# Optimization experiments

Hardware: AMD Instinct MI355X
Metric: run time of the kernel (lower is better)

The kernel has to match this reference:

```python
import jax, jax.numpy as jnp
import numpy as np

B, NQ, NP_, D = 4, 2048, 8192, 256
T, H = 10, 4  # num_tables, num_hash_functions -> hash code length T*H = 40


def setup_inputs() -> dict:
    key = jax.random.key(0)
    k1, k2, k3 = jax.random.split(key, 3)
    return {
        "query_points": jax.random.normal(k1, (B, NQ, D), dtype=jnp.float32),
        "points": jax.random.normal(k2, (B, NP_, D), dtype=jnp.float32),
        "proj": jax.random.normal(k3, (T * H, D), dtype=jnp.float32),  # projection_matrices
        "k": 16,
    }


def _hash(x, proj):
    # x: [B, N, D], proj: [T*H, D] -> binary hash [B, N, T*H]
    return (jnp.einsum('bnd,fd->bnf', x, proj) > 0).astype(jnp.float32)


def reference(query_points, points, proj, k):
    qh = _hash(query_points, proj)   # [B, Nq, F]
    ph = _hash(points, proj)         # [B, Np, F]
    # L1 cdist on {0,1}-valued vectors == Hamming: |a-b| = a + b - 2ab (exact in fp32).
    sq = qh.sum(-1)                  # [B, Nq]
    sp = ph.sum(-1)                  # [B, Np]
    dist = sq[:, :, None] + sp[:, None, :] - 2.0 * jnp.einsum('bqf,bpf->bqp', qh, ph)
    kk = min(int(k), points.shape[1])
    neg_vals, indices = jax.lax.top_k(-dist, kk)  # smallest-k distances
    return indices, -neg_vals
```

## Files before the change

kernel.cpp:

```cpp
#include <hip/hip_runtime.h>
#include <stdint.h>

#define B_  4
#define NQ_ 2048
#define NP_ 8192
#define D_  256
#define F_  40
#define K_  16

__global__ __launch_bounds__(512) void hash_kernel(
    const float* __restrict__ qp, const float* __restrict__ pp,
    const float* __restrict__ proj, uint64_t* __restrict__ qcodes,
    uint64_t* __restrict__ pcodes) {
  __shared__ float tile[64 * 260];
  int t = threadIdx.x;
  int v0 = blockIdx.x * 64;
  bool isQ = v0 < B_ * NQ_;
  const float* src =
      isQ ? (qp + (size_t)v0 * D_) : (pp + (size_t)(v0 - B_ * NQ_) * D_);
  const float4* src4 = (const float4*)src;

#pragma unroll
  for (int i = 0; i < 8; ++i) {
    float4 x = src4[i * 512 + t];
    int r = i * 8 + (t >> 6);
    int c = t & 63;
    *(float4*)&tile[r * 260 + 4 * c] = x;
  }
  __syncthreads();

  int lane = t & 63, w = t >> 6;
  int fbase = __builtin_amdgcn_readfirstlane(w * 5);
  const float* pj = proj + (size_t)fbase * 256;
  const float4* trow4 = (const float4*)&tile[lane * 260];

  float acc[5];
#pragma unroll
  for (int f = 0; f < 5; ++f) acc[f] = 0.0f;
#pragma unroll 8
  for (int d4 = 0; d4 < 64; ++d4) {
    float4 x4 = trow4[d4];
#pragma unroll
    for (int f = 0; f < 5; ++f) {
      acc[f] = fmaf(x4.x, pj[f * 256 + 4 * d4 + 0], acc[f]);
      acc[f] = fmaf(x4.y, pj[f * 256 + 4 * d4 + 1], acc[f]);
      acc[f] = fmaf(x4.z, pj[f * 256 + 4 * d4 + 2], acc[f]);
      acc[f] = fmaf(x4.w, pj[f * 256 + 4 * d4 + 3], acc[f]);
    }
  }
  unsigned bits = 0;
#pragma unroll
  for (int f = 0; f < 5; ++f)
    if (acc[f] > 0.0f) bits |= 1u << f;

  __syncthreads();
  unsigned short* cb = (unsigned short*)tile;
  cb[lane * 8 + w] = (unsigned short)bits;
  __syncthreads();
  if (w == 0) {
    uint64_t code = 0;
#pragma unroll
    for (int j = 0; j < 8; ++j)
      code |= (uint64_t)cb[lane * 8 + j] << (5 * j);
    int gv = v0 + lane;
    if (isQ) qcodes[gv] = code;
    else pcodes[gv - B_ * NQ_] = code;
  }
}

__global__ __launch_bounds__(512, 8) void select_kernel(
    const uint64_t* __restrict__ qcodes, const uint64_t* __restrict__ pcodes,
    float* __restrict__ outIdx, float* __restrict__ outDist) {
  __shared__ unsigned nib[8 * 1024];
  __shared__ unsigned keybuf[8][K_];

  int tid = threadIdx.x;
  int w = tid >> 6, lane = tid & 63;
  int qg = blockIdx.x * 8 + w;
  int bb = blockIdx.x >> 8;
  const ulonglong2* pb2 = (const ulonglong2*)(pcodes + (size_t)bb * NP_);
  uint64_t qc = qcodes[qg];
  unsigned* nibw = nib + w * 1024;
  const uint64_t M = 0x00FF00FF00FF00FFull;

  uint64_t cf = 0;
  unsigned accum = 0;
#pragma unroll 4
  for (int j2 = 0; j2 < 64; ++j2) {
    ulonglong2 pc = pb2[j2 * 64 + lane];
    unsigned d0 = (unsigned)__popcll(qc ^ pc.x);
    unsigned d1 = (unsigned)__popcll(qc ^ pc.y);
    unsigned c0 = d0 < 15u ? d0 : 15u;
    unsigned c1 = d1 < 15u ? d1 : 15u;
    accum |= (c0 | (c1 << 4)) << (8 * (j2 & 3));
    int r0 = (int)d0 - 8; r0 = r0 < 0 ? 0 : (r0 > 7 ? 7 : r0);
    int r1 = (int)d1 - 8; r1 = r1 < 0 ? 0 : (r1 > 7 ? 7 : r1);
    cf += (1ull << (r0 << 3)) + (1ull << (r1 << 3));
    if ((j2 & 3) == 3) {
      nibw[lane + 64 * (j2 >> 2)] = accum;
      accum = 0;
    }
  }
  uint64_t e = cf & M, o = (cf >> 8) & M;
#pragma unroll
  for (int s = 1; s < 64; s <<= 1) {
    e += __shfl_xor(e, s);
    o += __shfl_xor(o, s);
  }

  int t = 0;
  unsigned n_lt = 0;
  int rfound = -1;
  {
    unsigned cum = 0;
#pragma unroll
    for (int r = 0; r < 8; ++r) {
      unsigned c = (unsigned)(((r & 1) ? o : e) >> ((r >> 1) * 16)) & 0xFFFFu;
      if (rfound < 0 && cum + c >= K_) { rfound = r; t = 8 + r; n_lt = cum; }
      cum += c;
    }
  }
  uint64_t lmask = (1ull << lane) - 1;

  if (rfound >= 1 && rfound <= 6) {
    unsigned r_need = K_ - n_lt;
    unsigned cl = 0, ce = 0;
    unsigned ut = (unsigned)t;
#pragma unroll 4
    for (int k = 0; k < 16; ++k) {
      unsigned dw = nibw[lane + 64 * k];
#pragma unroll
      for (int b = 0; b < 4; ++b) {
        unsigned d0 = (dw >> (8 * b)) & 0xFu;
        unsigned d1 = (dw >> (8 * b + 4)) & 0xFu;
        int p0 = (4 * k + b) * 128 + 2 * lane;
        uint64_t m0 = __ballot(d0 < ut);
        uint64_t m1 = __ballot(d1 < ut);
        if (m0 | m1) {
          unsigned base = cl + (unsigned)__popcll(m0 & lmask) +
                          (unsigned)__popcll(m1 & lmask);
          if (d0 < ut) keybuf[w][base] = (d0 << 13) | (unsigned)p0;
          if (d1 < ut)
            keybuf[w][base + (unsigned)((m0 >> lane) & 1)] =
                (d1 << 13) | (unsigned)(p0 + 1);
          cl += (unsigned)__popcll(m0) + (unsigned)__popcll(m1);
        }
        if (ce < r_need) {
          uint64_t q0 = __ballot(d0 == ut);
          uint64_t q1 = __ballot(d1 == ut);
          if (q0 | q1) {
            unsigned b2 = ce + (unsigned)__popcll(q0 & lmask) +
                          (unsigned)__popcll(q1 & lmask);
            unsigned pos1 = b2 + (unsigned)((q0 >> lane) & 1);
            if (d0 == ut && b2 < r_need)
              keybuf[w][n_lt + b2] = (ut << 13) | (unsigned)p0;
            if (d1 == ut && pos1 < r_need)
              keybuf[w][n_lt + pos1] = (ut << 13) | (unsigned)(p0 + 1);
            ce += (unsigned)__popcll(q0) + (unsigned)__popcll(q1);
          }
        }
      }
    }
  } else {
    const uint64_t* pbl = pcodes + (size_t)bb * NP_;
    uint64_t c8 = 0;
#pragma unroll 4
    for (int j = 0; j < 64; ++j) {
      ulonglong2 pc = pb2[j * 64 + lane];
      int d0 = __popcll(qc ^ pc.x);
      int d1 = __popcll(qc ^ pc.y);
      c8 += (1ull << (d0 & 56)) + (1ull << (d1 & 56));
    }
    uint64_t e2 = c8 & M, o2 = (c8 >> 8) & M;
#pragma unroll
    for (int s = 1; s < 64; s <<= 1) {
      e2 += __shfl_xor(e2, s);
      o2 += __shfl_xor(o2, s);
    }
    int Bb = 0;
    unsigned nbefore = 0, cum = 0;
    bool found = false;
#pragma unroll
    for (int k2 = 0; k2 < 6; ++k2) {
      unsigned c = (unsigned)(((k2 & 1) ? o2 : e2) >> ((k2 >> 1) * 16)) & 0xFFFFu;
      if (!found && cum + c >= K_) { Bb = k2; nbefore = cum; found = true; }
      cum += c;
    }
    int base = Bb * 8;
    uint64_t cff = 0;
#pragma unroll 4
    for (int j = 0; j < 64; ++j) {
      ulonglong2 pc = pb2[j * 64 + lane];
      unsigned r0 = (unsigned)(__popcll(qc ^ pc.x) - base);
      unsigned r1 = (unsigned)(__popcll(qc ^ pc.y) - base);
      if (r0 < 8u) cff += 1ull << (r0 << 3);
      if (r1 < 8u) cff += 1ull << (r1 << 3);
    }
    uint64_t ef = cff & M, of = (cff >> 8) & M;
#pragma unroll
    for (int s = 1; s < 64; s <<= 1) {
      ef += __shfl_xor(ef, s);
      of += __shfl_xor(of, s);
    }
    unsigned cum2 = nbefore;
    bool f2 = false;
#pragma unroll
    for (int r = 0; r < 8; ++r) {
      unsigned c = (unsigned)(((r & 1) ? of : ef) >> ((r >> 1) * 16)) & 0xFFFFu;
      if (!f2 && cum2 + c >= K_) { t = base + r; n_lt = cum2; f2 = true; }
      cum2 += c;
    }
    unsigned r_need = K_ - n_lt;
    unsigned cl = 0, ce = 0;
    for (int j = 0; j < 128; ++j) {
      int p = j * 64 + lane;
      int d = __popcll(qc ^ pbl[p]);
      if (__any(d <= t)) {
        bool blt = (d < t), beq = (d == t);
        uint64_t mlt = __ballot(blt), meq = __ballot(beq);
        if (blt)
          keybuf[w][cl + (unsigned)__popcll(mlt & lmask)] =
              ((unsigned)d << 13) | (unsigned)p;
        if (beq) {
          unsigned pos = ce + (unsigned)__popcll(meq & lmask);
          if (pos < r_need)
            keybuf[w][n_lt + pos] = ((unsigned)d << 13) | (unsigned)p;
        }
        cl += (unsigned)__popcll(mlt);
        ce += (unsigned)__popcll(meq);
      }
    }
  }

  if (lane < K_) {
    unsigned my = keybuf[w][lane];
    int rank = 0;
#pragma unroll
    for (int jj = 0; jj < K_; ++jj) rank += (keybuf[w][jj] < my) ? 1 : 0;
    int off = qg * K_ + rank;
    outIdx[off]  = (float)(my & 8191u);
    outDist[off] = (float)(my >> 13);
  }
}

extern "C" void kernel_launch(void* const* d_in, const int* in_sizes, int n_in,
                              void* d_out, int out_size, void* d_ws, size_t ws_size,
                              hipStream_t stream) {
  const float* qp   = (const float*)d_in[0];
  const float* pp   = (const float*)d_in[1];
  const float* proj = (const float*)d_in[2];

  uint64_t* pcodes = (uint64_t*)d_ws;
  uint64_t* qcodes = pcodes + (size_t)B_ * NP_;

  float* outIdx  = (float*)d_out;
  float* outDist = outIdx + (size_t)B_ * NQ_ * K_;

  int total_vecs = B_ * (NQ_ + NP_);
  hash_kernel<<<total_vecs / 64, 512, 0, stream>>>(qp, pp, proj, qcodes, pcodes);
  select_kernel<<<B_ * NQ_ / 8, 512, 0, stream>>>(qcodes, pcodes, outIdx, outDist);
}
```

Before: 145.0 us.

## Double-buffer hash kernel input tiles in D-chunks to overlap loads with FMAs

The hash kernel no longer stages a full 64x256 float tile (about 66KB LDS) before computing. It now streams 64-column chunks into two small LDS buffers, loading chunk c+1 while computing on chunk c. The launch bounds also ask for 8 blocks per CU. The goal is to cut LDS use so more blocks are resident, and to hide global load latency behind the FMAs. The cost is extra barriers per chunk and more register pressure under the tighter launch bound.

```diff
diff --git a/kernel.cpp b/kernel.cpp
--- a/kernel.cpp
+++ b/kernel.cpp
@@ -8,11 +8,12 @@
 #define F_  40
 #define K_  16
 
-__global__ __launch_bounds__(512) void hash_kernel(
+__global__ __launch_bounds__(512, 8) void hash_kernel(
     const float* __restrict__ qp, const float* __restrict__ pp,
     const float* __restrict__ proj, uint64_t* __restrict__ qcodes,
     uint64_t* __restrict__ pcodes) {
-  __shared__ float tile[64 * 260];
+  __shared__ float buf[2][64][68];
+  __shared__ unsigned short cbuf[64][8];
   int t = threadIdx.x;
   int v0 = blockIdx.x * 64;
   bool isQ = v0 < B_ * NQ_;
@@ -20,48 +21,58 @@
       isQ ? (qp + (size_t)v0 * D_) : (pp + (size_t)(v0 - B_ * NQ_) * D_);
   const float4* src4 = (const float4*)src;
 
-#pragma unroll
-  for (int i = 0; i < 8; ++i) {
-    float4 x = src4[i * 512 + t];
-    int r = i * 8 + (t >> 6);
-    int c = t & 63;
-    *(float4*)&tile[r * 260 + 4 * c] = x;
-  }
-  __syncthreads();
-
   int lane = t & 63, w = t >> 6;
   int fbase = __builtin_amdgcn_readfirstlane(w * 5);
   const float* pj = proj + (size_t)fbase * 256;
-  const float4* trow4 = (const float4*)&tile[lane * 260];
+
+#define STAGE(c)                                              \
+  {                                                           \
+    _Pragma("unroll")                                         \
+    for (int i = 0; i < 2; ++i) {                             \
+      int idx = i * 512 + t;                                  \
+      int v = idx >> 4, f4 = idx & 15;                        \
+      float4 x = src4[v * 64 + (c) * 16 + f4];                \
+      *(float4*)&buf[(c) & 1][v][4 * f4] = x;                 \
+    }                                                         \
+  }
 
   float acc[5];
 #pragma unroll
   for (int f = 0; f < 5; ++f) acc[f] = 0.0f;
-#pragma unroll 8
-  for (int d4 = 0; d4 < 64; ++d4) {
-    float4 x4 = trow4[d4];
-#pragma unroll
-    for (int f = 0; f < 5; ++f) {
-      acc[f] = fmaf(x4.x, pj[f * 256 + 4 * d4 + 0], acc[f]);
-      acc[f] = fmaf(x4.y, pj[f * 256 + 4 * d4 + 1], acc[f]);
-      acc[f] = fmaf(x4.z, pj[f * 256 + 4 * d4 + 2], acc[f]);
-      acc[f] = fmaf(x4.w, pj[f * 256 + 4 * d4 + 3], acc[f]);
-    }
-  }
+
+  STAGE(0);
+  __syncthreads();
+#pragma unroll
+  for (int c = 0; c < 4; ++c) {
+    if (c < 3) STAGE(c + 1);
+    const float4* row4 = (const float4*)&buf[c & 1][lane][0];
+#pragma unroll
+    for (int d4 = 0; d4 < 16; ++d4) {
+      float4 x4 = row4[d4];
+#pragma unroll
+      for (int f = 0; f < 5; ++f) {
+        acc[f] = fmaf(x4.x, pj[f * 256 + c * 64 + 4 * d4 + 0], acc[f]);
+        acc[f] = fmaf(x4.y, pj[f * 256 + c * 64 + 4 * d4 + 1], acc[f]);
+        acc[f] = fmaf(x4.z, pj[f * 256 + c * 64 + 4 * d4 + 2], acc[f]);
+        acc[f] = fmaf(x4.w, pj[f * 256 + c * 64 + 4 * d4 + 3], acc[f]);
+      }
+    }
+    __syncthreads();
+  }
+#undef STAGE
+
   unsigned bits = 0;
 #pragma unroll
   for (int f = 0; f < 5; ++f)
     if (acc[f] > 0.0f) bits |= 1u << f;
 
-  __syncthreads();
-  unsigned short* cb = (unsigned short*)tile;
-  cb[lane * 8 + w] = (unsigned short)bits;
+  cbuf[lane][w] = (unsigned short)bits;
   __syncthreads();
   if (w == 0) {
     uint64_t code = 0;
 #pragma unroll
     for (int j = 0; j < 8; ++j)
-      code |= (uint64_t)cb[lane * 8 + j] << (5 * j);
+      code |= (uint64_t)cbuf[lane][j] << (5 * j);
     int gv = v0 + lane;
     if (isQ) qcodes[gv] = code;
     else pcodes[gv - B_ * NQ_] = code;
```

Result: faster. 141.5 us (-2.5%).
